# Performance work log

Measured on AMD Instinct MI355X. Metric: run time of the kernel, lower is better.

The kernel has to match this reference:

```python
import jax, jax.numpy as jnp
import numpy as np

N_PARTS = 24


def setup_inputs() -> dict:
    key = jax.random.key(0)
    k1, k2, k3, k4 = jax.random.split(key, 4)
    B, C, R = 8, 16, 512
    H = W = 512
    tex = jax.random.normal(k1, (B, C, R, R), dtype=jnp.float32)
    # iuv: channel 0 = part id in [0, 24] (0 == background), channels 1,2 = UV bytes in [0, 255]
    part = jax.random.randint(k2, (B, 1, H, W), 0, N_PARTS + 1, dtype=jnp.int32)
    uv = jax.random.randint(k3, (B, 2, H, W), 0, 256, dtype=jnp.int32)
    iuv = jnp.concatenate([part, uv], axis=1)
    lut = jax.random.uniform(k4, (N_PARTS, 256, 256, 2), dtype=jnp.float32)
    return {"tex": tex, "iuv": iuv, "lut": lut, "tex_res": R}


def reference(tex, iuv, lut, tex_res):
    # tex: [B, C, R, R], iuv: [B, 3, H, W] int, lut: [24, 256, 256, 2]
    B = tex.shape[0]
    mask = iuv[:, 0] > 0                                   # [B, H, W]
    i = jnp.clip(iuv[:, 0] - 1, 0, lut.shape[0] - 1)       # part index, clamped for masked-out pixels
    u = jnp.clip(iuv[:, 1].astype(jnp.float32) / 255.0, 0.0, 1.0)
    v = jnp.clip(iuv[:, 2].astype(jnp.float32) / 255.0, 0.0, 1.0)
    ui = jnp.round(u * 255.0).astype(jnp.int32)
    vi = jnp.round(v * 255.0).astype(jnp.int32)
    uv_smpl = lut[i, vi, ui]                               # [B, H, W, 2]
    u_I = jnp.round(uv_smpl[..., 0] * (tex_res - 1)).astype(jnp.int32)
    v_I = jnp.round((1.0 - uv_smpl[..., 1]) * (tex_res - 1)).astype(jnp.int32)
    b_idx = jnp.arange(B)[:, None, None]                   # [B, 1, 1]
    gathered = tex[b_idx, :, v_I, u_I]                     # [B, H, W, C]
    out = jnp.where(mask[..., None], gathered, jnp.zeros((), tex.dtype))
    return jnp.transpose(out, (0, 3, 1, 2))                # [B, C, H, W]
```

## Files before the change

kernel.cpp:

```cpp
#include <hip/hip_runtime.h>


#define N_PARTS 24

typedef float v4f __attribute__((ext_vector_type(4)));
typedef int   v4i __attribute__((ext_vector_type(4)));

__global__ __launch_bounds__(256) void dp_transpose_kernel(
    const float* __restrict__ tex,
    float*       __restrict__ texT)
{
    constexpr int C = 16, R = 512;
    constexpr size_t plane = (size_t)R * R;
    __shared__ float lds[16 * 516];

    const int tid = blockIdx.x;
    const int b  = tid >> 9;
    const int ty = tid & 511;
    const float* src = tex + (size_t)b * C * plane + (size_t)ty * R;
    const int t = threadIdx.x;

    #pragma unroll
    for (int k = 0; k < 8; ++k) {
        const int f  = k * 256 + t;
        const int c  = f >> 7;
        const int x4 = f & 127;
        const v4f v = __builtin_nontemporal_load(
            (const v4f*)(src + (size_t)c * plane + x4 * 4));
        *(v4f*)&lds[c * 516 + x4 * 4] = v;
    }
    __syncthreads();
    float* dst = texT + ((size_t)b * plane + (size_t)ty * R) * C;
    #pragma unroll
    for (int k = 0; k < 8; ++k) {
        const int f  = k * 256 + t;
        const int x  = f >> 2;
        const int c0 = (f & 3) * 4;
        v4f v;
        v.x = lds[(c0 + 0) * 516 + x];
        v.y = lds[(c0 + 1) * 516 + x];
        v.z = lds[(c0 + 2) * 516 + x];
        v.w = lds[(c0 + 3) * 516 + x];
        __builtin_nontemporal_store(v, (v4f*)(dst + (size_t)f * 4));
    }
}

__global__ __launch_bounds__(256) void dp_offsets_kernel(
    const int*   __restrict__ iuv,
    const float* __restrict__ lut,
    int*         __restrict__ offs,
    int R)
{
    constexpr int H = 512, W = 512;
    const float scale = (float)(R - 1);
    const size_t hw = (size_t)H * W;
    const int t = blockIdx.x * blockDim.x + threadIdx.x;
    const int pix4 = t * 4;
    const int b = pix4 >> 18;
    const int p = pix4 & (int)(hw - 1);

    const size_t ibase = (size_t)b * 3 * hw + p;
    const v4i p4 = __builtin_nontemporal_load((const v4i*)(iuv + ibase));
    const v4i u4 = __builtin_nontemporal_load((const v4i*)(iuv + ibase + hw));
    const v4i v4 = __builtin_nontemporal_load((const v4i*)(iuv + ibase + 2 * hw));

    const int parts[4] = {p4.x, p4.y, p4.z, p4.w};
    const int us[4]    = {u4.x, u4.y, u4.z, u4.w};
    const int vs[4]    = {v4.x, v4.y, v4.z, v4.w};

    v4i o4;
    #pragma unroll
    for (int j = 0; j < 4; ++j) {
        int i = parts[j] - 1;
        i = i < 0 ? 0 : (i > N_PARTS - 1 ? N_PARTS - 1 : i);
        const float fu = fminf(fmaxf((float)us[j] / 255.0f, 0.0f), 1.0f);
        const float fv = fminf(fmaxf((float)vs[j] / 255.0f, 0.0f), 1.0f);
        const int ui = (int)rintf(fu * 255.0f);
        const int vi = (int)rintf(fv * 255.0f);
        const float2 s = *(const float2*)(lut + (((size_t)i * 256 + vi) * 256 + ui) * 2);
        const int uI = (int)rintf(s.x * scale);
        const int vI = (int)rintf((1.0f - s.y) * scale);
        const int o = (parts[j] > 0) ? (vI * R + uI) : -1;
        if (j == 0) o4.x = o; else if (j == 1) o4.y = o;
        else if (j == 2) o4.z = o; else o4.w = o;
    }
    __builtin_nontemporal_store(o4, (v4i*)(offs + (size_t)b * hw + p));
}

__global__ __launch_bounds__(256) void dp_gatherT_kernel(
    const float* __restrict__ texT,
    const int*   __restrict__ offs,
    float*       __restrict__ out)
{
    constexpr int C = 16;
    constexpr size_t HW = 512 * 512;
    __shared__ float lds[4 * 1024];
    extern __shared__ float occupancy_pad[];

    const int b     = blockIdx.x & 7;
    const int inner = blockIdx.x >> 3;
    const int base  = inner * 1024;

    const int t    = threadIdx.x;
    const int lane = t & 63;
    const int wv   = t >> 6;

    const float* tb   = texT + (size_t)b * HW * C;
    const int*   obw  = offs + (size_t)b * HW + base + wv * 256;
    float*       outb = out  + (size_t)b * C * HW + base + wv * 256;
    float*       wlds = lds + wv * 1024;

    int o[4];
    #pragma unroll
    for (int i = 0; i < 4; ++i)
        o[i] = __builtin_nontemporal_load(obw + i * 64 + lane);

    v4f c0, c1, c2, c3;
    {
        const v4f* src = (const v4f*)(tb + (size_t)(o[0] >= 0 ? o[0] : 0) * C);
        c0 = src[0]; c1 = src[1]; c2 = src[2]; c3 = src[3];
    }

    #pragma unroll
    for (int iter = 0; iter < 4; ++iter) {
        v4f n0 = 0.f, n1 = 0.f, n2 = 0.f, n3 = 0.f;
        if (iter < 3) {
            const int on = o[iter + 1];
            const v4f* src = (const v4f*)(tb + (size_t)(on >= 0 ? on : 0) * C);
            n0 = src[0]; n1 = src[1]; n2 = src[2]; n3 = src[3];
        }

        if (o[iter] < 0) { c0 = 0.f; c1 = 0.f; c2 = 0.f; c3 = 0.f; }
        wlds[ 0 * 64 + lane] = c0.x;  wlds[ 1 * 64 + lane] = c0.y;
        wlds[ 2 * 64 + lane] = c0.z;  wlds[ 3 * 64 + lane] = c0.w;
        wlds[ 4 * 64 + lane] = c1.x;  wlds[ 5 * 64 + lane] = c1.y;
        wlds[ 6 * 64 + lane] = c1.z;  wlds[ 7 * 64 + lane] = c1.w;
        wlds[ 8 * 64 + lane] = c2.x;  wlds[ 9 * 64 + lane] = c2.y;
        wlds[10 * 64 + lane] = c2.z;  wlds[11 * 64 + lane] = c2.w;
        wlds[12 * 64 + lane] = c3.x;  wlds[13 * 64 + lane] = c3.y;
        wlds[14 * 64 + lane] = c3.z;  wlds[15 * 64 + lane] = c3.w;

        #pragma unroll
        for (int k = 0; k < 4; ++k) {
            const v4f v = *(const v4f*)&wlds[k * 256 + lane * 4];
            const int c = k * 4 + (lane >> 4);
            const int s = lane & 15;
            __builtin_nontemporal_store(
                v, (v4f*)(outb + (size_t)c * HW + iter * 64 + s * 4));
        }

        c0 = n0; c1 = n1; c2 = n2; c3 = n3;
    }
}

__global__ __launch_bounds__(256) void dp_gather_kernel(
    const float* __restrict__ tex,
    const int*   __restrict__ offs,
    float*       __restrict__ out,
    int R)
{
    constexpr int C = 16, H = 512, W = 512;
    const size_t hw    = (size_t)H * W;
    const size_t plane = (size_t)R * R;

    const int bid  = blockIdx.x;
    const int xcd  = bid & 7;
    const int slot = bid >> 3;
    const int pl_local = slot >> 8;
    const int inner    = slot & 255;
    const int pidx = xcd * 16 + pl_local;
    const int b = pidx >> 4;
    const int c = pidx & 15;

    const int px = inner * 1024 + threadIdx.x * 4;

    const int4 o4 = *(const int4*)(offs + (size_t)b * hw + px);
    const float* tc = tex + ((size_t)b * C + c) * plane;

    float4 r;
    r.x = (o4.x >= 0) ? tc[o4.x] : 0.0f;
    r.y = (o4.y >= 0) ? tc[o4.y] : 0.0f;
    r.z = (o4.z >= 0) ? tc[o4.z] : 0.0f;
    r.w = (o4.w >= 0) ? tc[o4.w] : 0.0f;

    *(float4*)(out + ((size_t)b * C + c) * hw + px) = r;
}

extern "C" void kernel_launch(void* const* d_in, const int* in_sizes, int n_in,
                              void* d_out, int out_size, void* d_ws, size_t ws_size,
                              hipStream_t stream) {
    const float* tex = (const float*)d_in[0];
    const int*   iuv = (const int*)d_in[1];
    const float* lut = (const float*)d_in[2];
    float*       out = (float*)d_out;

    constexpr int B = 8, C = 16, H = 512, W = 512;
    int R = 512;
    {
        long long pe = (long long)in_sizes[0] / (B * C);
        int r = 1; while ((long long)(r + 1) * (r + 1) <= pe) ++r;
        R = r;
    }

    const size_t texT_bytes = (size_t)B * R * R * C * sizeof(float);
    const size_t offs_bytes = (size_t)B * H * W * sizeof(int);

    if (R == 512 && ws_size >= texT_bytes + offs_bytes) {
        float* texT = (float*)d_ws;
        int*   offs = (int*)((char*)d_ws + texT_bytes);
        dp_transpose_kernel<<<dim3(4096), dim3(256), 0, stream>>>(tex, texT);
        dp_offsets_kernel<<<dim3(B * H * W / 4 / 256), dim3(256), 0, stream>>>(
            iuv, lut, offs, R);
        dp_gatherT_kernel<<<dim3(2048), dim3(256), 45056, stream>>>(
            texT, offs, out);
    } else if (ws_size >= offs_bytes) {
        int* offs = (int*)d_ws;
        dp_offsets_kernel<<<dim3(B * H * W / 4 / 256), dim3(256), 0, stream>>>(
            iuv, lut, offs, R);
        dp_gather_kernel<<<dim3(B * C * (H * W / 1024)), dim3(256), 0, stream>>>(
            tex, offs, out, R);
    }
}
```

Measured before the change: 338.8 us.

## Gather texels with four lanes per pixel and issue all loads up front

The gather kernel now loads each wave's 256 pixel offsets with one vector load into LDS. Each texel row is then fetched by four lanes, each reading 16 bytes, so every load instruction covers 16 pixels with coalesced 64-byte segments. All 16 gathers per lane are issued before any LDS transpose and store, which raises memory-level parallelism. The cost is more VGPR pressure (16 v4f values live at once) and extra LDS traffic, and the LDS write pattern in the transpose may cause bank conflicts.

Result: no change. 335.5 us (-1.0%).

```diff
diff --git a/kernel.cpp b/kernel.cpp
--- a/kernel.cpp
+++ b/kernel.cpp
@@ -95,6 +95,7 @@
     constexpr int C = 16;
     constexpr size_t HW = 512 * 512;
     __shared__ float lds[4 * 1024];
+    __shared__ int   olds[4 * 256];
     extern __shared__ float occupancy_pad[];
 
     const int b     = blockIdx.x & 7;
@@ -108,49 +109,62 @@
     const float* tb   = texT + (size_t)b * HW * C;
     const int*   obw  = offs + (size_t)b * HW + base + wv * 256;
     float*       outb = out  + (size_t)b * C * HW + base + wv * 256;
-    float*       wlds = lds + wv * 1024;
-
-    int o[4];
-    #pragma unroll
-    for (int i = 0; i < 4; ++i)
-        o[i] = __builtin_nontemporal_load(obw + i * 64 + lane);
-
-    v4f c0, c1, c2, c3;
+    float*       wlds = lds  + wv * 1024;
+    int*         wo   = olds + wv * 256;
+
     {
-        const v4f* src = (const v4f*)(tb + (size_t)(o[0] >= 0 ? o[0] : 0) * C);
-        c0 = src[0]; c1 = src[1]; c2 = src[2]; c3 = src[3];
-    }
-
-    #pragma unroll
-    for (int iter = 0; iter < 4; ++iter) {
-        v4f n0 = 0.f, n1 = 0.f, n2 = 0.f, n3 = 0.f;
-        if (iter < 3) {
-            const int on = o[iter + 1];
-            const v4f* src = (const v4f*)(tb + (size_t)(on >= 0 ? on : 0) * C);
-            n0 = src[0]; n1 = src[1]; n2 = src[2]; n3 = src[3];
-        }
-
-        if (o[iter] < 0) { c0 = 0.f; c1 = 0.f; c2 = 0.f; c3 = 0.f; }
-        wlds[ 0 * 64 + lane] = c0.x;  wlds[ 1 * 64 + lane] = c0.y;
-        wlds[ 2 * 64 + lane] = c0.z;  wlds[ 3 * 64 + lane] = c0.w;
-        wlds[ 4 * 64 + lane] = c1.x;  wlds[ 5 * 64 + lane] = c1.y;
-        wlds[ 6 * 64 + lane] = c1.z;  wlds[ 7 * 64 + lane] = c1.w;
-        wlds[ 8 * 64 + lane] = c2.x;  wlds[ 9 * 64 + lane] = c2.y;
-        wlds[10 * 64 + lane] = c2.z;  wlds[11 * 64 + lane] = c2.w;
-        wlds[12 * 64 + lane] = c3.x;  wlds[13 * 64 + lane] = c3.y;
-        wlds[14 * 64 + lane] = c3.z;  wlds[15 * 64 + lane] = c3.w;
-
-        #pragma unroll
-        for (int k = 0; k < 4; ++k) {
-            const v4f v = *(const v4f*)&wlds[k * 256 + lane * 4];
-            const int c = k * 4 + (lane >> 4);
-            const int s = lane & 15;
-            __builtin_nontemporal_store(
-                v, (v4f*)(outb + (size_t)c * HW + iter * 64 + s * 4));
-        }
-
-        c0 = n0; c1 = n1; c2 = n2; c3 = n3;
-    }
+        const v4i o4 = __builtin_nontemporal_load((const v4i*)(obw + lane * 4));
+        *(v4i*)&wo[lane * 4] = o4;
+    }
+
+    const int sub = lane >> 2;
+    const int q   = lane & 3;
+
+    v4f g00,g01,g02,g03, g10,g11,g12,g13, g20,g21,g22,g23, g30,g31,g32,g33;
+    int o00,o01,o02,o03, o10,o11,o12,o13, o20,o21,o22,o23, o30,o31,o32,o33;
+#define DP_LOAD(IT, J, GV, OV)                                               \
+    {                                                                        \
+        OV = wo[(IT) * 64 + (J) * 16 + sub];                                 \
+        const float* s_ = tb + (size_t)(OV >= 0 ? OV : 0) * C + q * 4;       \
+        GV = *(const v4f*)s_;                                                \
+    }
+    DP_LOAD(0,0,g00,o00) DP_LOAD(0,1,g01,o01) DP_LOAD(0,2,g02,o02) DP_LOAD(0,3,g03,o03)
+    DP_LOAD(1,0,g10,o10) DP_LOAD(1,1,g11,o11) DP_LOAD(1,2,g12,o12) DP_LOAD(1,3,g13,o13)
+    DP_LOAD(2,0,g20,o20) DP_LOAD(2,1,g21,o21) DP_LOAD(2,2,g22,o22) DP_LOAD(2,3,g23,o23)
+    DP_LOAD(3,0,g30,o30) DP_LOAD(3,1,g31,o31) DP_LOAD(3,2,g32,o32) DP_LOAD(3,3,g33,o33)
+#undef DP_LOAD
+
+#define DP_PUT(J, GV, OV)                                                    \
+    {                                                                        \
+        v4f v_ = GV;                                                         \
+        if (OV < 0) v_ = 0.f;                                                \
+        const int px_ = (J) * 16 + sub;                                      \
+        const int c0_ = q * 4;                                               \
+        wlds[(c0_ + 0) * 64 + px_] = v_.x;                                   \
+        wlds[(c0_ + 1) * 64 + px_] = v_.y;                                   \
+        wlds[(c0_ + 2) * 64 + px_] = v_.z;                                   \
+        wlds[(c0_ + 3) * 64 + px_] = v_.w;                                   \
+    }
+#define DP_STORE(IT)                                                         \
+    _Pragma("unroll")                                                        \
+    for (int k = 0; k < 4; ++k) {                                            \
+        const v4f v_ = *(const v4f*)&wlds[k * 256 + lane * 4];               \
+        const int c_ = k * 4 + (lane >> 4);                                  \
+        const int s_ = lane & 15;                                            \
+        __builtin_nontemporal_store(                                         \
+            v_, (v4f*)(outb + (size_t)c_ * HW + (IT) * 64 + s_ * 4));        \
+    }
+
+    DP_PUT(0,g00,o00) DP_PUT(1,g01,o01) DP_PUT(2,g02,o02) DP_PUT(3,g03,o03)
+    DP_STORE(0)
+    DP_PUT(0,g10,o10) DP_PUT(1,g11,o11) DP_PUT(2,g12,o12) DP_PUT(3,g13,o13)
+    DP_STORE(1)
+    DP_PUT(0,g20,o20) DP_PUT(1,g21,o21) DP_PUT(2,g22,o22) DP_PUT(3,g23,o23)
+    DP_STORE(2)
+    DP_PUT(0,g30,o30) DP_PUT(1,g31,o31) DP_PUT(2,g32,o32) DP_PUT(3,g33,o33)
+    DP_STORE(3)
+#undef DP_PUT
+#undef DP_STORE
 }
 
 __global__ __launch_bounds__(256) void dp_gather_kernel(
```
